# Kernel optimization log

Measured on AMD Instinct MI355X. Metric: run time of the kernel, lower is better.

## Reference

```python
import jax, jax.numpy as jnp
import numpy as np

N_NODES = 50000
N_EDGES = 800000
D = 128


def _sage_layer(x, src, dst, W_neigh, W_root, b):
    # mean aggregation of source features at destination nodes
    msgs = x[src]                                            # [E, D] gather
    agg = jax.ops.segment_sum(msgs, dst, num_segments=N_NODES)
    deg = jax.ops.segment_sum(jnp.ones((src.shape[0],), x.dtype), dst,
                              num_segments=N_NODES)
    agg = agg / jnp.maximum(deg, 1.0)[:, None]               # [N, D]
    return agg @ W_neigh + x @ W_root + b


def setup_inputs() -> dict:
    key = jax.random.key(0)
    ks = jax.random.split(key, 8)
    s = 1.0 / np.sqrt(D)
    return {
        "x": jax.random.normal(ks[0], (N_NODES, D), jnp.float32),
        "edge_index": jax.random.randint(ks[1], (2, N_EDGES), 0, N_NODES,
                                         dtype=jnp.int64),
        "W_neigh1": jax.random.normal(ks[2], (D, D), jnp.float32) * s,
        "W_root1": jax.random.normal(ks[3], (D, D), jnp.float32) * s,
        "b1": jnp.zeros((D,), jnp.float32),
        "W_neigh2": jax.random.normal(ks[4], (D, D), jnp.float32) * s,
        "W_root2": jax.random.normal(ks[5], (D, D), jnp.float32) * s,
        "b2": jnp.zeros((D,), jnp.float32),
    }


def reference(x, edge_index, W_neigh1, W_root1, b1, W_neigh2, W_root2, b2):
    src, dst = edge_index[0], edge_index[1]
    hid = jax.nn.relu(_sage_layer(x, src, dst, W_neigh1, W_root1, b1))
    out = jax.nn.relu(_sage_layer(hid, src, dst, W_neigh2, W_root2, b2))
    return out
```

## Files before the change

### kernel.cpp

```cpp
#include <hip/hip_runtime.h>

#define N_NODES 50000
#define N_EDGES 800000
#define D 128
#define NBINS 196
#define BCAP 5120

typedef __attribute__((ext_vector_type(8))) short bf16x8;
typedef __attribute__((ext_vector_type(4))) float f32x4;

__device__ __forceinline__ unsigned short f2bf(float f) {
    unsigned u = __float_as_uint(f);
    unsigned r = (u + 0x7FFFu + ((u >> 16) & 1u)) >> 16;
    return (unsigned short)r;
}
__device__ __forceinline__ float bf2f(unsigned short h) {
    return __uint_as_float(((unsigned)h) << 16);
}

#define CVT_BLKS 3125
#define PACK_BLKS 128
#define BINA_BLKS 391

__device__ __forceinline__ void pack_one(const float* __restrict__ Wn,
                                         const float* __restrict__ Wr,
                                         ushort* __restrict__ Wp, int t) {
    int k = t >> 7, c = t & 127;
    float v = (k < 128) ? Wn[k * 128 + c] : Wr[(k - 128) * 128 + c];
    int ks = k >> 5, g = (k >> 3) & 3, i = k & 7;
    Wp[(((ks * 128 + c) * 4 + g) << 3) + i] = f2bf(v);
}

__global__ __launch_bounds__(256) void k_main(const float* __restrict__ x,
                                              ushort* __restrict__ xb,
                                              const float* __restrict__ Wn1,
                                              const float* __restrict__ Wr1,
                                              ushort* __restrict__ Wp1,
                                              const float* __restrict__ Wn2,
                                              const float* __restrict__ Wr2,
                                              ushort* __restrict__ Wp2,
                                              const int* __restrict__ src,
                                              const int* __restrict__ dst,
                                              int* __restrict__ binCnt,
                                              unsigned* __restrict__ binned) {
    __shared__ int lc[NBINS];
    int b = blockIdx.x;
    if (b < CVT_BLKS) {
        int i = b * 256 + threadIdx.x;
        const float4* p = (const float4*)(x + (size_t)i * 8);
        float4 a = p[0], c = p[1];
        uint4 o;
        o.x = (unsigned)f2bf(a.x) | ((unsigned)f2bf(a.y) << 16);
        o.y = (unsigned)f2bf(a.z) | ((unsigned)f2bf(a.w) << 16);
        o.z = (unsigned)f2bf(c.x) | ((unsigned)f2bf(c.y) << 16);
        o.w = (unsigned)f2bf(c.z) | ((unsigned)f2bf(c.w) << 16);
        *(uint4*)(xb + (size_t)i * 8) = o;
    } else if (b < CVT_BLKS + PACK_BLKS) {
        int t = (b - CVT_BLKS) * 256 + threadIdx.x;
        pack_one(Wn1, Wr1, Wp1, t);
        pack_one(Wn2, Wr2, Wp2, t);
    } else {
        const int tid = threadIdx.x;
        const int base = (b - CVT_BLKS - PACK_BLKS) * 2048;
        if (tid < NBINS) lc[tid] = 0;
        __syncthreads();
        int s[8], d[8];
        #pragma unroll
        for (int k = 0; k < 8; k++) {
            int i = base + k * 256 + tid;
            if (i < N_EDGES) {
                s[k] = src[i];
                d[k] = dst[i];
                atomicAdd(&lc[d[k] >> 8], 1);
            } else d[k] = -1;
        }
        __syncthreads();
        if (tid < NBINS) {
            int c = lc[tid];
            lc[tid] = c ? atomicAdd(&binCnt[tid], c) : 0;
        }
        __syncthreads();
        #pragma unroll
        for (int k = 0; k < 8; k++) {
            if (d[k] >= 0) {
                int bin = d[k] >> 8;
                int pos = atomicAdd(&lc[bin], 1);
                if (pos < BCAP)
                    binned[(size_t)bin * BCAP + pos] =
                        (unsigned)s[k] | ((unsigned)(d[k] & 255) << 16);
            }
        }
    }
}

__global__ __launch_bounds__(256) void k_binB(const unsigned* __restrict__ binned,
                                              const int* __restrict__ binCnt,
                                              int2* __restrict__ row,
                                              ushort* __restrict__ edge_src) {
    __shared__ int cnt[256];
    __shared__ int cur[256];
    __shared__ int ws4[4];
    const int tid = threadIdx.x, lane = tid & 63, w = tid >> 6;
    const int b = blockIdx.x;
    const int node0 = b << 8;
    int nNodes = N_NODES - node0; if (nNodes > 256) nNodes = 256;
    int ecnt = binCnt[b]; if (ecnt > BCAP) ecnt = BCAP;
    const unsigned* eb = binned + (size_t)b * BCAP;
    cnt[tid] = 0;
    __syncthreads();
    for (int e = tid; e < ecnt; e += 256)
        atomicAdd(&cnt[(eb[e] >> 16) & 255], 1);
    __syncthreads();
    int v = cnt[tid];
    int incl = v;
    #pragma unroll
    for (int off = 1; off < 64; off <<= 1) {
        int t = __shfl_up(incl, off);
        if (lane >= off) incl += t;
    }
    if (lane == 63) ws4[w] = incl;
    __syncthreads();
    int wo = 0;
    if (w > 0) wo += ws4[0];
    if (w > 1) wo += ws4[1];
    if (w > 2) wo += ws4[2];
    int excl = wo + incl - v;
    cur[tid] = excl;
    if (tid < nNodes) {
        int2 r; r.x = b * BCAP + excl; r.y = v;
        row[node0 + tid] = r;
    }
    __syncthreads();
    for (int e = tid; e < ecnt; e += 256) {
        unsigned rec = eb[e];
        int pos = atomicAdd(&cur[(rec >> 16) & 255], 1);
        edge_src[(size_t)b * BCAP + pos] = (ushort)(rec & 0xffffu);
    }
}

__global__ __launch_bounds__(256) void k_agg(const ushort* __restrict__ xb,
                                             const int2* __restrict__ row,
                                             const ushort* __restrict__ edge_src,
                                             ushort* __restrict__ aggb) {
    int node = (blockIdx.x * blockDim.x + threadIdx.x) >> 6;
    int lane = threadIdx.x & 63;
    if (node >= N_NODES) return;
    int2 bc = row[node];
    const int beg = bc.x, cn = bc.y, end = bc.x + bc.y;
    const int g  = lane >> 4;
    const int c8 = (lane & 15) * 8;
    float acc[8] = {};
    if (cn > 0) {
        for (int e = beg; e < end; e += 16) {
            int idx = e + (lane & 15);
            int ids = edge_src[idx < end ? idx : end - 1];
            #pragma unroll
            for (int u = 0; u < 4; u++) {
                int ee = e + u * 4 + g;
                float sc = ee < end ? 1.f : 0.f;
                int sid = __shfl(ids, u * 4 + g);
                bf16x8 v = *(const bf16x8*)&xb[(size_t)sid * D + c8];
                #pragma unroll
                for (int j = 0; j < 8; j++)
                    acc[j] = fmaf(bf2f((unsigned short)v[j]), sc, acc[j]);
            }
        }
    }
    #pragma unroll
    for (int j = 0; j < 8; j++) acc[j] += __shfl_xor(acc[j], 16);
    #pragma unroll
    for (int j = 0; j < 8; j++) acc[j] += __shfl_xor(acc[j], 32);
    if (lane < 16) {
        float inv = 1.0f / (float)(cn > 1 ? cn : 1);
        uint4 o;
        o.x = (unsigned)f2bf(acc[0] * inv) | ((unsigned)f2bf(acc[1] * inv) << 16);
        o.y = (unsigned)f2bf(acc[2] * inv) | ((unsigned)f2bf(acc[3] * inv) << 16);
        o.z = (unsigned)f2bf(acc[4] * inv) | ((unsigned)f2bf(acc[5] * inv) << 16);
        o.w = (unsigned)f2bf(acc[6] * inv) | ((unsigned)f2bf(acc[7] * inv) << 16);
        *(uint4*)&aggb[(size_t)node * D + c8] = o;
    }
}

template <int OUT_F32>
__global__ __launch_bounds__(128) void k_gemm(const ushort* __restrict__ Ab,
                                              const ushort* __restrict__ Xb,
                                              const ushort* __restrict__ Wp,
                                              const float* __restrict__ bias,
                                              void* __restrict__ outv) {
    const int lane = threadIdx.x & 63;
    const int wid  = threadIdx.x >> 6;
    const int row0 = blockIdx.x * 64;
    const int col0 = wid * 64;
    const int r = lane & 15, g = lane >> 4;

    f32x4 acc[4][4] = {};
    #pragma unroll
    for (int ks = 0; ks < 8; ks++) {
        const ushort* As = (ks < 4) ? Ab : Xb;
        const int kk = (ks & 3) * 32 + 8 * g;
        bf16x8 a[4], b[4];
        #pragma unroll
        for (int rf = 0; rf < 4; rf++) {
            int rr = row0 + rf * 16 + r;
            if (rr > N_NODES - 1) rr = N_NODES - 1;
            a[rf] = *(const bf16x8*)&As[(size_t)rr * D + kk];
        }
        #pragma unroll
        for (int cf = 0; cf < 4; cf++) {
            int c = col0 + cf * 16 + r;
            b[cf] = *(const bf16x8*)&Wp[(((size_t)ks * 128 + c) * 4 + g) * 8];
        }
        #pragma unroll
        for (int rf = 0; rf < 4; rf++)
            #pragma unroll
            for (int cf = 0; cf < 4; cf++)
                acc[rf][cf] = __builtin_amdgcn_mfma_f32_16x16x32_bf16(
                    a[rf], b[cf], acc[rf][cf], 0, 0, 0);
    }
    float bv[4];
    #pragma unroll
    for (int cf = 0; cf < 4; cf++) bv[cf] = bias[col0 + cf * 16 + r];
    #pragma unroll
    for (int rf = 0; rf < 4; rf++) {
        #pragma unroll
        for (int j = 0; j < 4; j++) {
            int rowi = row0 + rf * 16 + g * 4 + j;
            if (rowi < N_NODES) {
                #pragma unroll
                for (int cf = 0; cf < 4; cf++) {
                    float v = fmaxf(acc[rf][cf][j] + bv[cf], 0.f);
                    int col = col0 + cf * 16 + r;
                    if (OUT_F32) ((float*)outv)[(size_t)rowi * D + col] = v;
                    else ((ushort*)outv)[(size_t)rowi * D + col] = f2bf(v);
                }
            }
        }
    }
}

extern "C" void kernel_launch(void* const* d_in, const int* in_sizes, int n_in,
                              void* d_out, int out_size, void* d_ws, size_t ws_size,
                              hipStream_t stream) {
    const float* x   = (const float*)d_in[0];
    const int*   ei  = (const int*)d_in[1];
    const float* Wn1 = (const float*)d_in[2];
    const float* Wr1 = (const float*)d_in[3];
    const float* b1  = (const float*)d_in[4];
    const float* Wn2 = (const float*)d_in[5];
    const float* Wr2 = (const float*)d_in[6];
    const float* b2  = (const float*)d_in[7];
    float* out = (float*)d_out;

    const int* src = ei;
    const int* dst = ei + N_EDGES;

    const size_t bfb = (size_t)N_NODES * D * 2;
    const size_t packb = 256 * 128 * 2;
    auto au = [](size_t v) { return (v + 255) & ~(size_t)255; };

    char* w = (char*)d_ws;
    size_t o = 0;
    ushort* aggb = (ushort*)(w + o);     o += au(bfb);
    ushort* hb   = (ushort*)(w + o);     o += au(bfb);
    ushort* edge_src = (ushort*)(w + o); o += au((size_t)NBINS * BCAP * 2);
    ushort* Wp2  = (ushort*)(w + o);     o += au(packb);

    char* q = (char*)d_out;
    size_t p = 0;
    ushort* xb = (ushort*)(q + p);         p += au(bfb);
    unsigned* binned = (unsigned*)(q + p); p += au((size_t)NBINS * BCAP * 4);
    int2* row = (int2*)(q + p);            p += au((size_t)N_NODES * 8);
    ushort* Wp1 = (ushort*)(q + p);        p += au(packb);
    int* binCnt = (int*)(q + p);

    hipMemsetAsync(binCnt, 0, NBINS * sizeof(int), stream);
    k_main<<<CVT_BLKS + PACK_BLKS + BINA_BLKS, 256, 0, stream>>>(
        x, xb, Wn1, Wr1, Wp1, Wn2, Wr2, Wp2, src, dst, binCnt, binned);
    k_binB<<<NBINS, 256, 0, stream>>>(binned, binCnt, row, edge_src);

    const int aggGrid  = (N_NODES * 64) / 256;
    const int gemmGrid = (N_NODES + 63) / 64;

    k_agg<<<aggGrid, 256, 0, stream>>>(xb, row, edge_src, aggb);
    k_gemm<0><<<gemmGrid, 128, 0, stream>>>(aggb, xb, Wp1, b1, hb);
    k_agg<<<aggGrid, 256, 0, stream>>>(hb, row, edge_src, aggb);
    k_gemm<1><<<gemmGrid, 128, 0, stream>>>(aggb, hb, Wp2, b2, out);
}
```

Baseline: 129.2 us.

## Split neighbor aggregation into four feature-column slices per node

The aggregation kernel now gives each node four wavefronts, each covering a 32-column slice of the feature row. Within a slice, 8 edges are gathered at once with 8-byte loads instead of 4 edges with 16-byte loads. The grid grows fourfold, and each slice reads the edge index list again. The aim is more memory-level parallelism and less per-wave serial latency on high-degree nodes, at the cost of redundant index reads, narrower loads and more wavefronts.

```diff
diff --git a/kernel.cpp b/kernel.cpp
--- a/kernel.cpp
+++ b/kernel.cpp
@@ -5,6 +5,8 @@
 #define D 128
 #define NBINS 196
 #define BCAP 5120
+#define NSLICE 4
+#define SLICE_BLKS 12500
 
 typedef __attribute__((ext_vector_type(8))) short bf16x8;
 typedef __attribute__((ext_vector_type(4))) float f32x4;
@@ -138,46 +140,47 @@
     }
 }
 
-__global__ __launch_bounds__(256) void k_agg(const ushort* __restrict__ xb,
-                                             const int2* __restrict__ row,
-                                             const ushort* __restrict__ edge_src,
-                                             ushort* __restrict__ aggb) {
-    int node = (blockIdx.x * blockDim.x + threadIdx.x) >> 6;
-    int lane = threadIdx.x & 63;
-    if (node >= N_NODES) return;
+__global__ __launch_bounds__(256) void k_aggs(const ushort* __restrict__ xb,
+                                              const int2* __restrict__ row,
+                                              const ushort* __restrict__ edge_src,
+                                              ushort* __restrict__ aggb) {
+    const int bx = blockIdx.x;
+    const int slice = bx / SLICE_BLKS;
+    const int node = (bx - slice * SLICE_BLKS) * 4 + (threadIdx.x >> 6);
+    const int lane = threadIdx.x & 63;
     int2 bc = row[node];
-    const int beg = bc.x, cn = bc.y, end = bc.x + bc.y;
-    const int g  = lane >> 4;
-    const int c8 = (lane & 15) * 8;
-    float acc[8] = {};
-    if (cn > 0) {
-        for (int e = beg; e < end; e += 16) {
-            int idx = e + (lane & 15);
-            int ids = edge_src[idx < end ? idx : end - 1];
-            #pragma unroll
-            for (int u = 0; u < 4; u++) {
-                int ee = e + u * 4 + g;
-                float sc = ee < end ? 1.f : 0.f;
-                int sid = __shfl(ids, u * 4 + g);
-                bf16x8 v = *(const bf16x8*)&xb[(size_t)sid * D + c8];
-                #pragma unroll
-                for (int j = 0; j < 8; j++)
-                    acc[j] = fmaf(bf2f((unsigned short)v[j]), sc, acc[j]);
-            }
-        }
-    }
-    #pragma unroll
-    for (int j = 0; j < 8; j++) acc[j] += __shfl_xor(acc[j], 16);
-    #pragma unroll
-    for (int j = 0; j < 8; j++) acc[j] += __shfl_xor(acc[j], 32);
-    if (lane < 16) {
+    const int beg = bc.x, cn = bc.y, end = beg + cn;
+    const int g  = lane >> 3;
+    const int c4 = (lane & 7) * 4 + slice * 32;
+    float a0 = 0.f, a1 = 0.f, a2 = 0.f, a3 = 0.f;
+    for (int e = beg; e < end; e += 16) {
+        int idx = e + (lane & 15);
+        int ids = edge_src[idx < end ? idx : end - 1];
+        #pragma unroll
+        for (int h = 0; h < 2; h++) {
+            int ee = e + h * 8 + g;
+            float sc = ee < end ? 1.f : 0.f;
+            int sid = __shfl(ids, h * 8 + g);
+            uint2 v = *(const uint2*)&xb[(size_t)sid * D + c4];
+            a0 = fmaf(bf2f((unsigned short)(v.x & 0xffffu)), sc, a0);
+            a1 = fmaf(bf2f((unsigned short)(v.x >> 16)), sc, a1);
+            a2 = fmaf(bf2f((unsigned short)(v.y & 0xffffu)), sc, a2);
+            a3 = fmaf(bf2f((unsigned short)(v.y >> 16)), sc, a3);
+        }
+    }
+    #pragma unroll
+    for (int off = 8; off < 64; off <<= 1) {
+        a0 += __shfl_xor(a0, off);
+        a1 += __shfl_xor(a1, off);
+        a2 += __shfl_xor(a2, off);
+        a3 += __shfl_xor(a3, off);
+    }
+    if (lane < 8) {
         float inv = 1.0f / (float)(cn > 1 ? cn : 1);
-        uint4 o;
-        o.x = (unsigned)f2bf(acc[0] * inv) | ((unsigned)f2bf(acc[1] * inv) << 16);
-        o.y = (unsigned)f2bf(acc[2] * inv) | ((unsigned)f2bf(acc[3] * inv) << 16);
-        o.z = (unsigned)f2bf(acc[4] * inv) | ((unsigned)f2bf(acc[5] * inv) << 16);
-        o.w = (unsigned)f2bf(acc[6] * inv) | ((unsigned)f2bf(acc[7] * inv) << 16);
-        *(uint4*)&aggb[(size_t)node * D + c8] = o;
+        uint2 o;
+        o.x = (unsigned)f2bf(a0 * inv) | ((unsigned)f2bf(a1 * inv) << 16);
+        o.y = (unsigned)f2bf(a2 * inv) | ((unsigned)f2bf(a3 * inv) << 16);
+        *(uint2*)&aggb[(size_t)node * D + lane * 4 + slice * 32] = o;
     }
 }
 
@@ -278,11 +281,11 @@
         x, xb, Wn1, Wr1, Wp1, Wn2, Wr2, Wp2, src, dst, binCnt, binned);
     k_binB<<<NBINS, 256, 0, stream>>>(binned, binCnt, row, edge_src);
 
-    const int aggGrid  = (N_NODES * 64) / 256;
+    const int aggGrid  = NSLICE * SLICE_BLKS;
     const int gemmGrid = (N_NODES + 63) / 64;
 
-    k_agg<<<aggGrid, 256, 0, stream>>>(xb, row, edge_src, aggb);
+    k_aggs<<<aggGrid, 256, 0, stream>>>(xb, row, edge_src, aggb);
     k_gemm<0><<<gemmGrid, 128, 0, stream>>>(aggb, xb, Wp1, b1, hb);
-    k_agg<<<aggGrid, 256, 0, stream>>>(hb, row, edge_src, aggb);
+    k_aggs<<<aggGrid, 256, 0, stream>>>(hb, row, edge_src, aggb);
     k_gemm<1><<<gemmGrid, 128, 0, stream>>>(aggb, hb, Wp2, b2, out);
 }
```

New measurement: 195.2 us. 51.1% more time.
